# Kernel tuning notes

Measured on AMD Instinct MI355X. Metric: run time of the kernel, lower is better.

## Reference

```python
import jax, jax.numpy as jnp
import numpy as np

NUM_GROUPS = 4
NUM_HEADS = 4
EPS = 1e-6

def group_norm(x, scale, bias):
    # x: [B, C, L]
    b, c, l = x.shape
    g = NUM_GROUPS
    xg = x.reshape(b, g, (c // g) * l)
    mean = xg.mean(axis=-1, keepdims=True)
    var = xg.var(axis=-1, keepdims=True)
    xg = (xg - mean) * jax.lax.rsqrt(var + EPS)
    xn = xg.reshape(b, c, l)
    return xn * scale[None, :, None] + bias[None, :, None]

def conv1x1(x, w, b):
    # x: [B, C_in, L], w: [C_out, C_in], b: [C_out]
    return jnp.einsum('oc,bcl->bol', w, x) + b[None, :, None]

def setup_inputs() -> dict:
    key = jax.random.key(0)
    ks = jax.random.split(key, 11)
    B, C, L = 8, 512, 2048
    x = jax.random.normal(ks[0], (B, C, L), dtype=jnp.float32)
    s = 1.0 / np.sqrt(C)
    return {
        'x': x,
        'gn_scale': jnp.ones((C,), jnp.float32),
        'gn_bias': jnp.zeros((C,), jnp.float32),
        'wq': jax.random.normal(ks[1], (C, C), jnp.float32) * s,
        'bq': jnp.zeros((C,), jnp.float32),
        'wk': jax.random.normal(ks[2], (C, C), jnp.float32) * s,
        'bk': jnp.zeros((C,), jnp.float32),
        'wv': jax.random.normal(ks[3], (C, C), jnp.float32) * s,
        'bv': jnp.zeros((C,), jnp.float32),
        'wo': jax.random.normal(ks[4], (C, C), jnp.float32) * s,
        'bo': jnp.zeros((C,), jnp.float32),
    }

def reference(x, gn_scale, gn_bias, wq, bq, wk, bk, wv, bv, wo, bo):
    b, c, l = x.shape
    nh = NUM_HEADS
    hd = c // nh
    h_ = group_norm(x, gn_scale, gn_bias)
    q = conv1x1(h_, wq, bq).reshape(b, nh, hd, l)
    k = conv1x1(h_, wk, bk).reshape(b, nh, hd, l)
    v = conv1x1(h_, wv, bv).reshape(b, nh, hd, l)
    # scores: [b, nh, l(query), l(key)]
    w_ = jnp.einsum('bhdq,bhdk->bhqk', q, k) * (hd ** -0.5)
    w_ = jax.nn.softmax(w_, axis=-1)
    # attn: [b, nh, l(query), hd]
    attn = jnp.einsum('bhqk,bhdk->bhqd', w_, v)
    attn = attn.transpose(0, 1, 3, 2).reshape(b, c, l)
    out = conv1x1(attn, wo, bo)
    return x + out
```

## Files before the change

kernel.cpp:

```cpp
#include <hip/hip_runtime.h>


typedef unsigned short u16;
typedef unsigned int   u32;
typedef unsigned long long u64;
typedef __attribute__((ext_vector_type(8)))  short          bf16x8;
typedef __attribute__((ext_vector_type(4)))  float          f32x4;
typedef __attribute__((ext_vector_type(4)))  unsigned int   u32x4;
typedef __attribute__((ext_vector_type(8)))  unsigned short u16x8;

#define MFMA16(a, b, c) __builtin_amdgcn_mfma_f32_16x16x32_bf16((a), (b), (c), 0, 0, 0)

#define WAIT_VM6         3958
#define WAIT_VM4_LGKM0    116
#define BARRIER() __builtin_amdgcn_s_barrier()

__device__ __forceinline__ u16 f2bf(float f) {
    union { float f; unsigned int i; } cv;
    cv.f = f;
    unsigned int u = cv.i;
    u += 0x7fffu + ((u >> 16) & 1);
    return (u16)(u >> 16);
}
__device__ __forceinline__ u32 fbits(float f) {
    union { float f; unsigned int i; } cv; cv.f = f; return cv.i;
}

__device__ __forceinline__ void async16(const u16* g, u16* l) {
    __builtin_amdgcn_global_load_lds(
        (const __attribute__((address_space(1))) unsigned int*)g,
        (__attribute__((address_space(3))) unsigned int*)l, 16, 0, 0);
}

#define BATCH 8
#define CCH   512
#define LEN   2048
#define NGRP  4
#define NHEAD 4
#define HD    128
#define GSIZE (128 * 2048)

__global__ __launch_bounds__(256) void wcvt_k(const float* __restrict__ w0,
                                              const float* __restrict__ w1,
                                              const float* __restrict__ w2,
                                              const float* __restrict__ w3,
                                              u16* __restrict__ dst) {
    const int mat = blockIdx.y;
    const float* src = (mat == 0) ? w0 : (mat == 1) ? w1 : (mat == 2) ? w2 : w3;
    const size_t base = (size_t)blockIdx.x * 2048 + (size_t)threadIdx.x * 8;
    f32x4 a = *(const f32x4*)(src + base);
    f32x4 b = *(const f32x4*)(src + base + 4);
    u16x8 o;
    for (int u = 0; u < 4; ++u) { o[u] = f2bf(a[u]); o[u + 4] = f2bf(b[u]); }
    *(u16x8*)(dst + (size_t)mat * 262144 + base) = o;
}

__global__ __launch_bounds__(256) void gn_stats_k(const float* __restrict__ x,
                                                  float* __restrict__ stats) {
    const int bid   = blockIdx.x;
    const int grp   = bid >> 3;
    const int chunk = bid & 7;
    const int b = grp >> 2, g = grp & 3;
    const float* base = x + ((size_t)(b * CCH + g * 128 + chunk * 16)) * LEN;

    float s = 0.f, ss = 0.f;
    for (int i = 0; i < 32; ++i) {
        int cid = threadIdx.x + i * 256;
        f32x4 dv = *(const f32x4*)(base + (size_t)cid * 4);
        for (int u = 0; u < 4; ++u) { s += dv[u]; ss += dv[u] * dv[u]; }
    }
    for (int m = 1; m < 64; m <<= 1) {
        s  += __shfl_xor(s,  m, 64);
        ss += __shfl_xor(ss, m, 64);
    }
    __shared__ float red[8];
    int wid = threadIdx.x >> 6, lane = threadIdx.x & 63;
    if (lane == 0) { red[wid * 2] = s; red[wid * 2 + 1] = ss; }
    __syncthreads();
    if (threadIdx.x == 0) {
        float ts  = red[0] + red[2] + red[4] + red[6];
        float tss = red[1] + red[3] + red[5] + red[7];
        atomicAdd(&stats[grp * 2],     ts);
        atomicAdd(&stats[grp * 2 + 1], tss);
    }
}

__global__ __launch_bounds__(256) void gn_apply_k(const float* __restrict__ x,
                                                  const float* __restrict__ gns,
                                                  const float* __restrict__ gnb,
                                                  const float* __restrict__ stats,
                                                  u16* __restrict__ hT) {
    __shared__ u16 Ts[64 * 72];
    const int b = blockIdx.z, c0 = blockIdx.y * 64, l0 = blockIdx.x * 64;
    const int g = c0 >> 7;
    const int tid = threadIdx.x;

    float sum   = stats[(b * NGRP + g) * 2];
    float sumsq = stats[(b * NGRP + g) * 2 + 1];
    const float invN = 1.f / (float)GSIZE;
    float mean = sum * invN;
    float var  = sumsq * invN - mean * mean;
    float rstd = rsqrtf(var + 1e-6f);

    for (int i = 0; i < 4; ++i) {
        int cid = tid + i * 256;
        int row = cid >> 4, c4 = cid & 15;
        int c = c0 + row;
        float sc = gns[c] * rstd;
        float bi = gnb[c] - mean * sc;
        f32x4 dv = *(const f32x4*)(x + ((size_t)(b * CCH + c)) * LEN + l0 + c4 * 4);
        for (int u = 0; u < 4; ++u)
            Ts[row * 72 + c4 * 4 + u] = f2bf(dv[u] * sc + bi);
    }
    __syncthreads();
    for (int i = 0; i < 2; ++i) {
        int cid = tid + i * 256;
        int lrow = cid >> 3, c8 = cid & 7;
        u16x8 ov;
        for (int u = 0; u < 8; ++u) ov[u] = Ts[(c8 * 8 + u) * 72 + lrow];
        *(u16x8*)(hT + ((size_t)b * LEN + l0 + lrow) * CCH + c0 + c8 * 8) = ov;
    }
}

template <int MODE>
__global__ __launch_bounds__(256, 2) void gemm_k(const u16* __restrict__ A0,
                                                 const u16* __restrict__ B0,
                                                 const u16* __restrict__ B1,
                                                 const float* __restrict__ bias0,
                                                 const float* __restrict__ bias1,
                                                 const float* __restrict__ resid,
                                                 void* __restrict__ out0v,
                                                 u16* __restrict__ out1) {
    __shared__ u16 As[2][128 * 64];
    __shared__ u16 Bs[2][128 * 64];
    const int b  = blockIdx.z;
    const int n0 = blockIdx.x * 128;
    const int m0 = blockIdx.y * 128;
    const int tid = threadIdx.x;
    const int lane = tid & 63, wid = tid >> 6;
    const int quad = lane >> 4, l15 = lane & 15;
    const int wm = (wid & 1) * 64, wn = (wid >> 1) * 64;

    const u16* Arow;
    if constexpr (MODE == 0) Arow = A0 + ((size_t)b * LEN + m0) * 512;
    else                     Arow = A0 + (size_t)m0 * 512;

    const u16* Brow;
    int col0 = 0;
    if constexpr (MODE == 0) {
        if (n0 < 512) { Brow = B0 + (size_t)n0 * 512;         col0 = n0; }
        else          { Brow = B1 + (size_t)(n0 - 512) * 512;  col0 = n0 - 512; }
    } else {
        Brow = B0 + ((size_t)b * LEN + n0) * 512;
    }

    f32x4 acc[4][4] = {};
    const int srl = lane >> 3, scl = lane & 7;

#pragma unroll
    for (int i = 0; i < 4; ++i) {
        int rloc = wid * 32 + i * 8 + srl;
        int lc = scl ^ (rloc & 7);
        async16(Arow + (size_t)rloc * 512 + lc * 8, &As[0][(wid * 32 + i * 8) * 64]);
        async16(Brow + (size_t)rloc * 512 + lc * 8, &Bs[0][(wid * 32 + i * 8) * 64]);
    }
    __syncthreads();

    for (int kk = 0; kk < 8; ++kk) {
        const int p = kk & 1;
        if (kk < 7) {
            const int k0n = (kk + 1) * 64;
#pragma unroll
            for (int i = 0; i < 4; ++i) {
                int rloc = wid * 32 + i * 8 + srl;
                int lc = scl ^ (rloc & 7);
                async16(Arow + (size_t)rloc * 512 + k0n + lc * 8,
                        &As[1 - p][(wid * 32 + i * 8) * 64]);
                async16(Brow + (size_t)rloc * 512 + k0n + lc * 8,
                        &Bs[1 - p][(wid * 32 + i * 8) * 64]);
            }
        }
#pragma unroll
        for (int ks = 0; ks < 2; ++ks) {
            bf16x8 af[4], bfr[4];
            for (int t = 0; t < 4; ++t) {
                int ra = wm + t * 16 + l15, rb = wn + t * 16 + l15;
                af[t]  = *(const bf16x8*)(&As[p][ra * 64 + (((ks * 4 + quad) ^ (ra & 7))) * 8]);
                bfr[t] = *(const bf16x8*)(&Bs[p][rb * 64 + (((ks * 4 + quad) ^ (rb & 7))) * 8]);
            }
            for (int mt = 0; mt < 4; ++mt)
                for (int nt = 0; nt < 4; ++nt)
                    acc[mt][nt] = MFMA16(af[mt], bfr[nt], acc[mt][nt]);
        }
        __syncthreads();
    }

    if constexpr (MODE == 0) {
        const float* biasp = (n0 < 512) ? (bias0 + col0) : (bias1 + col0);
        u16* outp = (n0 < 512) ? (u16*)out0v : out1;
        for (int nt = 0; nt < 4; ++nt) {
            int nl = wn + nt * 16 + l15;
            float bv_ = biasp[nl];
            for (int mt = 0; mt < 4; ++mt)
                for (int r = 0; r < 4; ++r) {
                    int ml = wm + mt * 16 + quad * 4 + r;
                    size_t idx = ((size_t)b * LEN + m0 + ml) * 512 + col0 + nl;
                    outp[idx] = f2bf(acc[mt][nt][r] + bv_);
                }
        }
    } else {
        for (int mt = 0; mt < 4; ++mt)
            for (int r = 0; r < 4; ++r) {
                int ml = wm + mt * 16 + quad * 4 + r;
                float bv_ = bias0[m0 + ml];
                for (int nt = 0; nt < 4; ++nt) {
                    int nl = wn + nt * 16 + l15;
                    size_t idx = ((size_t)(b * 512 + m0 + ml)) * LEN + n0 + nl;
                    float val = acc[mt][nt][r] + bv_;
                    if constexpr (MODE == 2) {
                        ((float*)out0v)[idx] = val + resid[idx];
                    } else {
                        ((u16*)out0v)[idx] = f2bf(val);
                    }
                }
            }
    }
}

__global__ __launch_bounds__(512, 4) void attn_k(const u16* __restrict__ qT,
                                                 const u16* __restrict__ kT,
                                                 const u16* __restrict__ v,
                                                 u16* __restrict__ attnT) {
    __shared__ u16 Ks[2][64 * 128];
    __shared__ u16 Vs[2][128 * 64];
    const int b = blockIdx.z, h = blockIdx.y;
    const int i0 = blockIdx.x * 128;
    const int tid = threadIdx.x, lane = tid & 63, wid = tid >> 6;
    const int quad = lane >> 4, l15 = lane & 15;
    const int mrow = wid * 16 + l15;

    bf16x8 qa[4];
    for (int ks = 0; ks < 4; ++ks)
        qa[ks] = *(const bf16x8*)(qT + ((size_t)b * LEN + i0 + mrow) * 512 + h * HD +
                                  ks * 32 + quad * 8);

    float mst = -3.0e38f, lst = 0.f;
    f32x4 oacc[8] = {};

    const float SL2E = 0.08838834764831845f * 1.4426950408889634f;

    const u16* kbase = kT + ((size_t)b * LEN) * 512 + h * HD;
    const u16* vbase = v + ((size_t)(b * CCH + h * HD)) * LEN;

    const u16* kgp[2];
    const u16* vgp[2];
    int krow[2], vrow[2];
#pragma unroll
    for (int i = 0; i < 2; ++i) {
        int rk = wid * 8 + i * 4 + (lane >> 4);
        krow[i] = wid * 8 + i * 4;
        kgp[i] = kbase + (size_t)rk * 512 + ((lane & 15) ^ (rk & 7)) * 8;
        int rv = wid * 16 + i * 8 + (lane >> 3);
        vrow[i] = wid * 16 + i * 8;
        vgp[i] = vbase + (size_t)rv * LEN + ((lane & 7) ^ (rv & 7)) * 8;
    }

#pragma unroll
    for (int i = 0; i < 2; ++i) {
        async16(kgp[i], &Ks[0][krow[i] * 128]);
        async16(vgp[i], &Vs[0][vrow[i] * 64]);
        kgp[i] += 64 * 512;
        vgp[i] += 64;
    }

    for (int jt = 0; jt < 32; ++jt) {
        const int p = jt & 1;

#pragma unroll
        for (int i = 0; i < 2; ++i) {
            async16(kgp[i], &Ks[1 - p][krow[i] * 128]);
            async16(vgp[i], &Vs[1 - p][vrow[i] * 64]);
        }
        if (jt < 30) {
#pragma unroll
            for (int i = 0; i < 2; ++i) { kgp[i] += 64 * 512; vgp[i] += 64; }
        }

        __builtin_amdgcn_s_waitcnt(WAIT_VM6);
        BARRIER();

        f32x4 st[4] = {};
#pragma unroll
        for (int jtn = 0; jtn < 4; ++jtn) {
            int r = jtn * 16 + l15;
            for (int ks = 0; ks < 4; ++ks) {
                bf16x8 kf = *(const bf16x8*)(&Ks[p][r * 128 + ((ks * 4 + quad) ^ (r & 7)) * 8]);
                st[jtn] = MFMA16(kf, qa[ks], st[jtn]);
            }
        }

        float rm = -3.0e38f;
        for (int jtn = 0; jtn < 4; ++jtn)
            for (int r = 0; r < 4; ++r) rm = fmaxf(rm, st[jtn][r]);
        rm *= SL2E;
        rm = fmaxf(rm, __shfl_xor(rm, 16, 64));
        rm = fmaxf(rm, __shfl_xor(rm, 32, 64));
        float mnew  = fmaxf(mst, rm);
        float alpha = __builtin_amdgcn_exp2f(mst - mnew);
        mst = mnew;
        float rs = 0.f;
        for (int jtn = 0; jtn < 4; ++jtn)
            for (int r = 0; r < 4; ++r) {
                float pv_ = __builtin_amdgcn_exp2f(st[jtn][r] * SL2E - mnew);
                st[jtn][r] = pv_;
                rs += pv_;
            }
        rs += __shfl_xor(rs, 16, 64);
        rs += __shfl_xor(rs, 32, 64);
        lst = lst * alpha + rs;

        if (__ballot(alpha != 1.0f) != 0ull) {
            float av[4];
            for (int r = 0; r < 4; ++r) av[r] = __shfl(alpha, quad * 4 + r, 16);
            for (int dt = 0; dt < 8; ++dt)
                for (int r = 0; r < 4; ++r) oacc[dt][r] *= av[r];
        }

        __builtin_amdgcn_s_waitcnt(WAIT_VM4_LGKM0);
        BARRIER();

        {
            int m = mrow;
#pragma unroll
            for (int jtn = 0; jtn < 4; ++jtn) {
                u64 packed =  (u64)((fbits(st[jtn][0]) + 0x8000u) >> 16)
                           | ((u64)((fbits(st[jtn][1]) + 0x8000u) >> 16) << 16)
                           | ((u64)((fbits(st[jtn][2]) + 0x8000u) >> 16) << 32)
                           | ((u64)((fbits(st[jtn][3]) + 0x8000u) >> 16) << 48);
                int pc = (jtn * 2 + (quad >> 1)) ^ (m & 7);
                *(u64*)(&Ks[p][m * 64 + pc * 8 + (quad & 1) * 4]) = packed;
            }
        }

#pragma unroll
        for (int ks = 0; ks < 2; ++ks) {
            bf16x8 pf = *(const bf16x8*)(&Ks[p][mrow * 64 + ((ks * 4 + quad) ^ (mrow & 7)) * 8]);
            for (int dt = 0; dt < 8; ++dt) {
                int d = dt * 16 + l15;
                bf16x8 vf = *(const bf16x8*)(&Vs[p][d * 64 + ((ks * 4 + quad) ^ (d & 7)) * 8]);
                oacc[dt] = MFMA16(pf, vf, oacc[dt]);
            }
        }

        __builtin_amdgcn_s_waitcnt(WAIT_VM4_LGKM0);
        BARRIER();
    }

    float inv = 1.f / lst;
    float iv[4];
    for (int r = 0; r < 4; ++r) iv[r] = __shfl(inv, quad * 4 + r, 16);
    for (int r = 0; r < 4; ++r) {
        int m = i0 + wid * 16 + quad * 4 + r;
        for (int dt = 0; dt < 8; ++dt) {
            int d = dt * 16 + l15;
            attnT[((size_t)b * LEN + m) * 512 + h * HD + d] = f2bf(oacc[dt][r] * iv[r]);
        }
    }
}

extern "C" void kernel_launch(void* const* d_in, const int* in_sizes, int n_in,
                              void* d_out, int out_size, void* d_ws, size_t ws_size,
                              hipStream_t stream) {
    const float* x   = (const float*)d_in[0];
    const float* gns = (const float*)d_in[1];
    const float* gnb = (const float*)d_in[2];
    const float* wq  = (const float*)d_in[3];
    const float* bq  = (const float*)d_in[4];
    const float* wk  = (const float*)d_in[5];
    const float* bk  = (const float*)d_in[6];
    const float* wv  = (const float*)d_in[7];
    const float* bv  = (const float*)d_in[8];
    const float* wo  = (const float*)d_in[9];
    const float* bo  = (const float*)d_in[10];
    float* out = (float*)d_out;

    const size_t NEL = (size_t)BATCH * CCH * LEN;
    float* stats = (float*)d_ws;
    u16* wcat  = (u16*)((char*)d_ws + 256);
    u16* hT    = wcat + 4 * 262144;
    u16* qT    = hT + NEL;
    u16* kT    = qT + NEL;
    u16* vbuf  = kT + NEL;
    u16* attnT = hT;

    const u16* wq_bf = wcat;
    const u16* wk_bf = wcat + 262144;
    const u16* wv_bf = wcat + 2 * 262144;
    const u16* wo_bf = wcat + 3 * 262144;

    hipMemsetAsync(d_ws, 0, 256, stream);
    wcvt_k<<<dim3(128, 4), 256, 0, stream>>>(wq, wk, wv, wo, wcat);
    gn_stats_k<<<256, 256, 0, stream>>>(x, stats);
    gn_apply_k<<<dim3(32, 8, 8), 256, 0, stream>>>(x, gns, gnb, stats, hT);
    gemm_k<0><<<dim3(8, 16, 8), 256, 0, stream>>>(hT, wq_bf, wk_bf, bq, bk, nullptr, qT, kT);
    gemm_k<1><<<dim3(16, 4, 8), 256, 0, stream>>>(wv_bf, hT, nullptr, bv, nullptr, nullptr, vbuf, nullptr);
    attn_k<<<dim3(16, 4, 8), 512, 0, stream>>>(qT, kT, vbuf, attnT);
    gemm_k<2><<<dim3(16, 4, 8), 256, 0, stream>>>(wo_bf, attnT, nullptr, bo, nullptr, x, out, nullptr);
}
```

Baseline: 271.7 us.

## Merge prep and QKV GEMM launches, remap attention blocks per XCD

Merges the weight-conversion and group-norm statistics kernels into one launch, and merges the QK and V projection GEMMs into a single 1536-block launch that picks its mode from the block index. It also flattens the attention grid so that each XCD (blockIdx & 7) handles four whole (batch, head) pairs, which is meant to keep K/V reuse inside one L2. The goal is fewer launches and better L2 locality. The trade-off is some divergent setup code and a fixed mapping that assumes 8 XCDs.

```diff
diff --git a/kernel.cpp b/kernel.cpp
--- a/kernel.cpp
+++ b/kernel.cpp
@@ -40,48 +40,50 @@
 #define HD    128
 #define GSIZE (128 * 2048)
 
-__global__ __launch_bounds__(256) void wcvt_k(const float* __restrict__ w0,
+__global__ __launch_bounds__(256) void prep_k(const float* __restrict__ x,
+                                              float* __restrict__ stats,
+                                              const float* __restrict__ w0,
                                               const float* __restrict__ w1,
                                               const float* __restrict__ w2,
                                               const float* __restrict__ w3,
                                               u16* __restrict__ dst) {
-    const int mat = blockIdx.y;
-    const float* src = (mat == 0) ? w0 : (mat == 1) ? w1 : (mat == 2) ? w2 : w3;
-    const size_t base = (size_t)blockIdx.x * 2048 + (size_t)threadIdx.x * 8;
-    f32x4 a = *(const f32x4*)(src + base);
-    f32x4 b = *(const f32x4*)(src + base + 4);
-    u16x8 o;
-    for (int u = 0; u < 4; ++u) { o[u] = f2bf(a[u]); o[u + 4] = f2bf(b[u]); }
-    *(u16x8*)(dst + (size_t)mat * 262144 + base) = o;
-}
-
-__global__ __launch_bounds__(256) void gn_stats_k(const float* __restrict__ x,
-                                                  float* __restrict__ stats) {
-    const int bid   = blockIdx.x;
-    const int grp   = bid >> 3;
-    const int chunk = bid & 7;
-    const int b = grp >> 2, g = grp & 3;
-    const float* base = x + ((size_t)(b * CCH + g * 128 + chunk * 16)) * LEN;
-
-    float s = 0.f, ss = 0.f;
-    for (int i = 0; i < 32; ++i) {
-        int cid = threadIdx.x + i * 256;
-        f32x4 dv = *(const f32x4*)(base + (size_t)cid * 4);
-        for (int u = 0; u < 4; ++u) { s += dv[u]; ss += dv[u] * dv[u]; }
-    }
-    for (int m = 1; m < 64; m <<= 1) {
-        s  += __shfl_xor(s,  m, 64);
-        ss += __shfl_xor(ss, m, 64);
-    }
-    __shared__ float red[8];
-    int wid = threadIdx.x >> 6, lane = threadIdx.x & 63;
-    if (lane == 0) { red[wid * 2] = s; red[wid * 2 + 1] = ss; }
-    __syncthreads();
-    if (threadIdx.x == 0) {
-        float ts  = red[0] + red[2] + red[4] + red[6];
-        float tss = red[1] + red[3] + red[5] + red[7];
-        atomicAdd(&stats[grp * 2],     ts);
-        atomicAdd(&stats[grp * 2 + 1], tss);
+    const int bid = blockIdx.x;
+    if (bid < 256) {
+        const int grp   = bid >> 3;
+        const int chunk = bid & 7;
+        const int b = grp >> 2, g = grp & 3;
+        const float* base = x + ((size_t)(b * CCH + g * 128 + chunk * 16)) * LEN;
+
+        float s = 0.f, ss = 0.f;
+        for (int i = 0; i < 32; ++i) {
+            int cid = threadIdx.x + i * 256;
+            f32x4 dv = *(const f32x4*)(base + (size_t)cid * 4);
+            for (int u = 0; u < 4; ++u) { s += dv[u]; ss += dv[u] * dv[u]; }
+        }
+        for (int m = 1; m < 64; m <<= 1) {
+            s  += __shfl_xor(s,  m, 64);
+            ss += __shfl_xor(ss, m, 64);
+        }
+        __shared__ float red[8];
+        int wid = threadIdx.x >> 6, lane = threadIdx.x & 63;
+        if (lane == 0) { red[wid * 2] = s; red[wid * 2 + 1] = ss; }
+        __syncthreads();
+        if (threadIdx.x == 0) {
+            float ts  = red[0] + red[2] + red[4] + red[6];
+            float tss = red[1] + red[3] + red[5] + red[7];
+            atomicAdd(&stats[grp * 2],     ts);
+            atomicAdd(&stats[grp * 2 + 1], tss);
+        }
+    } else {
+        const int wb = bid - 256;
+        const int mat = wb >> 7, chunk = wb & 127;
+        const float* src = (mat == 0) ? w0 : (mat == 1) ? w1 : (mat == 2) ? w2 : w3;
+        const size_t base = (size_t)chunk * 2048 + (size_t)threadIdx.x * 8;
+        f32x4 a = *(const f32x4*)(src + base);
+        f32x4 b2 = *(const f32x4*)(src + base + 4);
+        u16x8 o;
+        for (int u = 0; u < 4; ++u) { o[u] = f2bf(a[u]); o[u + 4] = f2bf(b2[u]); }
+        *(u16x8*)(dst + (size_t)mat * 262144 + base) = o;
     }
 }
 
@@ -122,15 +124,113 @@
     }
 }
 
-template <int MODE>
-__global__ __launch_bounds__(256, 2) void gemm_k(const u16* __restrict__ A0,
-                                                 const u16* __restrict__ B0,
-                                                 const u16* __restrict__ B1,
-                                                 const float* __restrict__ bias0,
-                                                 const float* __restrict__ bias1,
-                                                 const float* __restrict__ resid,
-                                                 void* __restrict__ out0v,
-                                                 u16* __restrict__ out1) {
+__global__ __launch_bounds__(256, 2) void gemm01_k(const u16* __restrict__ hT,
+                                                   const u16* __restrict__ wq_bf,
+                                                   const u16* __restrict__ wk_bf,
+                                                   const u16* __restrict__ wv_bf,
+                                                   const float* __restrict__ bq,
+                                                   const float* __restrict__ bk,
+                                                   const float* __restrict__ bv,
+                                                   u16* __restrict__ qT,
+                                                   u16* __restrict__ kT,
+                                                   u16* __restrict__ vbuf) {
+    __shared__ u16 As[2][128 * 64];
+    __shared__ u16 Bs[2][128 * 64];
+    const int bid = blockIdx.x;
+    const bool mode0 = (bid < 1024);
+    int b, m0, n0;
+    const u16 *Arow, *Brow;
+    if (mode0) {
+        b = bid >> 7; m0 = ((bid >> 3) & 15) * 128; n0 = (bid & 7) * 128;
+        Arow = hT + ((size_t)b * LEN + m0) * 512;
+        Brow = (n0 < 512) ? (wq_bf + (size_t)n0 * 512)
+                          : (wk_bf + (size_t)(n0 - 512) * 512);
+    } else {
+        int bid2 = bid - 1024;
+        b = bid2 >> 6; m0 = ((bid2 >> 4) & 3) * 128; n0 = (bid2 & 15) * 128;
+        Arow = wv_bf + (size_t)m0 * 512;
+        Brow = hT + ((size_t)b * LEN + n0) * 512;
+    }
+
+    const int tid = threadIdx.x;
+    const int lane = tid & 63, wid = tid >> 6;
+    const int quad = lane >> 4, l15 = lane & 15;
+    const int wm = (wid & 1) * 64, wn = (wid >> 1) * 64;
+
+    f32x4 acc[4][4] = {};
+    const int srl = lane >> 3, scl = lane & 7;
+
+#pragma unroll
+    for (int i = 0; i < 4; ++i) {
+        int rloc = wid * 32 + i * 8 + srl;
+        int lc = scl ^ (rloc & 7);
+        async16(Arow + (size_t)rloc * 512 + lc * 8, &As[0][(wid * 32 + i * 8) * 64]);
+        async16(Brow + (size_t)rloc * 512 + lc * 8, &Bs[0][(wid * 32 + i * 8) * 64]);
+    }
+    __syncthreads();
+
+    for (int kk = 0; kk < 8; ++kk) {
+        const int p = kk & 1;
+        if (kk < 7) {
+            const int k0n = (kk + 1) * 64;
+#pragma unroll
+            for (int i = 0; i < 4; ++i) {
+                int rloc = wid * 32 + i * 8 + srl;
+                int lc = scl ^ (rloc & 7);
+                async16(Arow + (size_t)rloc * 512 + k0n + lc * 8,
+                        &As[1 - p][(wid * 32 + i * 8) * 64]);
+                async16(Brow + (size_t)rloc * 512 + k0n + lc * 8,
+                        &Bs[1 - p][(wid * 32 + i * 8) * 64]);
+            }
+        }
+#pragma unroll
+        for (int ks = 0; ks < 2; ++ks) {
+            bf16x8 af[4], bfr[4];
+            for (int t = 0; t < 4; ++t) {
+                int ra = wm + t * 16 + l15, rb = wn + t * 16 + l15;
+                af[t]  = *(const bf16x8*)(&As[p][ra * 64 + (((ks * 4 + quad) ^ (ra & 7))) * 8]);
+                bfr[t] = *(const bf16x8*)(&Bs[p][rb * 64 + (((ks * 4 + quad) ^ (rb & 7))) * 8]);
+            }
+            for (int mt = 0; mt < 4; ++mt)
+                for (int nt = 0; nt < 4; ++nt)
+                    acc[mt][nt] = MFMA16(af[mt], bfr[nt], acc[mt][nt]);
+        }
+        __syncthreads();
+    }
+
+    if (mode0) {
+        const int col0 = (n0 < 512) ? n0 : n0 - 512;
+        const float* biasp = ((n0 < 512) ? bq : bk) + col0;
+        u16* outp = (n0 < 512) ? qT : kT;
+        for (int nt = 0; nt < 4; ++nt) {
+            int nl = wn + nt * 16 + l15;
+            float bv_ = biasp[nl];
+            for (int mt = 0; mt < 4; ++mt)
+                for (int r = 0; r < 4; ++r) {
+                    int ml = wm + mt * 16 + quad * 4 + r;
+                    size_t idx = ((size_t)b * LEN + m0 + ml) * 512 + col0 + nl;
+                    outp[idx] = f2bf(acc[mt][nt][r] + bv_);
+                }
+        }
+    } else {
+        for (int mt = 0; mt < 4; ++mt)
+            for (int r = 0; r < 4; ++r) {
+                int ml = wm + mt * 16 + quad * 4 + r;
+                float bv_ = bv[m0 + ml];
+                for (int nt = 0; nt < 4; ++nt) {
+                    int nl = wn + nt * 16 + l15;
+                    size_t idx = ((size_t)(b * 512 + m0 + ml)) * LEN + n0 + nl;
+                    vbuf[idx] = f2bf(acc[mt][nt][r] + bv_);
+                }
+            }
+    }
+}
+
+__global__ __launch_bounds__(256, 2) void gemm2_k(const u16* __restrict__ A0,
+                                                  const u16* __restrict__ B0,
+                                                  const float* __restrict__ bias0,
+                                                  const float* __restrict__ resid,
+                                                  float* __restrict__ out0) {
     __shared__ u16 As[2][128 * 64];
     __shared__ u16 Bs[2][128 * 64];
     const int b  = blockIdx.z;
@@ -141,18 +241,8 @@
     const int quad = lane >> 4, l15 = lane & 15;
     const int wm = (wid & 1) * 64, wn = (wid >> 1) * 64;
 
-    const u16* Arow;
-    if constexpr (MODE == 0) Arow = A0 + ((size_t)b * LEN + m0) * 512;
-    else                     Arow = A0 + (size_t)m0 * 512;
-
-    const u16* Brow;
-    int col0 = 0;
-    if constexpr (MODE == 0) {
-        if (n0 < 512) { Brow = B0 + (size_t)n0 * 512;         col0 = n0; }
-        else          { Brow = B1 + (size_t)(n0 - 512) * 512;  col0 = n0 - 512; }
-    } else {
-        Brow = B0 + ((size_t)b * LEN + n0) * 512;
-    }
+    const u16* Arow = A0 + (size_t)m0 * 512;
+    const u16* Brow = B0 + ((size_t)b * LEN + n0) * 512;
 
     f32x4 acc[4][4] = {};
     const int srl = lane >> 3, scl = lane & 7;
@@ -195,36 +285,16 @@
         __syncthreads();
     }
 
-    if constexpr (MODE == 0) {
-        const float* biasp = (n0 < 512) ? (bias0 + col0) : (bias1 + col0);
-        u16* outp = (n0 < 512) ? (u16*)out0v : out1;
-        for (int nt = 0; nt < 4; ++nt) {
-            int nl = wn + nt * 16 + l15;
-            float bv_ = biasp[nl];
-            for (int mt = 0; mt < 4; ++mt)
-                for (int r = 0; r < 4; ++r) {
-                    int ml = wm + mt * 16 + quad * 4 + r;
-                    size_t idx = ((size_t)b * LEN + m0 + ml) * 512 + col0 + nl;
-                    outp[idx] = f2bf(acc[mt][nt][r] + bv_);
-                }
-        }
-    } else {
-        for (int mt = 0; mt < 4; ++mt)
-            for (int r = 0; r < 4; ++r) {
-                int ml = wm + mt * 16 + quad * 4 + r;
-                float bv_ = bias0[m0 + ml];
-                for (int nt = 0; nt < 4; ++nt) {
-                    int nl = wn + nt * 16 + l15;
-                    size_t idx = ((size_t)(b * 512 + m0 + ml)) * LEN + n0 + nl;
-                    float val = acc[mt][nt][r] + bv_;
-                    if constexpr (MODE == 2) {
-                        ((float*)out0v)[idx] = val + resid[idx];
-                    } else {
-                        ((u16*)out0v)[idx] = f2bf(val);
-                    }
-                }
-            }
-    }
+    for (int mt = 0; mt < 4; ++mt)
+        for (int r = 0; r < 4; ++r) {
+            int ml = wm + mt * 16 + quad * 4 + r;
+            float bv_ = bias0[m0 + ml];
+            for (int nt = 0; nt < 4; ++nt) {
+                int nl = wn + nt * 16 + l15;
+                size_t idx = ((size_t)(b * 512 + m0 + ml)) * LEN + n0 + nl;
+                out0[idx] = acc[mt][nt][r] + bv_ + resid[idx];
+            }
+        }
 }
 
 __global__ __launch_bounds__(512, 4) void attn_k(const u16* __restrict__ qT,
@@ -233,8 +303,13 @@
                                                  u16* __restrict__ attnT) {
     __shared__ u16 Ks[2][64 * 128];
     __shared__ u16 Vs[2][128 * 64];
-    const int b = blockIdx.z, h = blockIdx.y;
-    const int i0 = blockIdx.x * 128;
+    const int bid = blockIdx.x;
+    const int xcd = bid & 7, slot = bid >> 3;
+    const int bh  = xcd * 4 + (slot >> 4);
+    const int qt  = slot & 15;
+    const int b = bh >> 2, h = bh & 3;
+    const int i0 = qt * 128;
+
     const int tid = threadIdx.x, lane = tid & 63, wid = tid >> 6;
     const int quad = lane >> 4, l15 = lane & 15;
     const int mrow = wid * 16 + l15;
@@ -399,11 +474,9 @@
     const u16* wo_bf = wcat + 3 * 262144;
 
     hipMemsetAsync(d_ws, 0, 256, stream);
-    wcvt_k<<<dim3(128, 4), 256, 0, stream>>>(wq, wk, wv, wo, wcat);
-    gn_stats_k<<<256, 256, 0, stream>>>(x, stats);
+    prep_k<<<768, 256, 0, stream>>>(x, stats, wq, wk, wv, wo, wcat);
     gn_apply_k<<<dim3(32, 8, 8), 256, 0, stream>>>(x, gns, gnb, stats, hT);
-    gemm_k<0><<<dim3(8, 16, 8), 256, 0, stream>>>(hT, wq_bf, wk_bf, bq, bk, nullptr, qT, kT);
-    gemm_k<1><<<dim3(16, 4, 8), 256, 0, stream>>>(wv_bf, hT, nullptr, bv, nullptr, nullptr, vbuf, nullptr);
-    attn_k<<<dim3(16, 4, 8), 512, 0, stream>>>(qT, kT, vbuf, attnT);
-    gemm_k<2><<<dim3(16, 4, 8), 256, 0, stream>>>(wo_bf, attnT, nullptr, bo, nullptr, x, out, nullptr);
-}
+    gemm01_k<<<1536, 256, 0, stream>>>(hT, wq_bf, wk_bf, wv_bf, bq, bk, bv, qT, kT, vbuf);
+    attn_k<<<512, 512, 0, stream>>>(qT, kT, vbuf, attnT);
+    gemm2_k<<<dim3(16, 4, 8), 256, 0, stream>>>(wo_bf, attnT, bo, x, out);
+}
```

New measurement: 268.8 us. Within noise of the previous version (-1.1%).
